# Performance work log

Measured on AMD Instinct MI355X. Metric: run time of the kernel, lower is better.

The kernel has to match this reference:

```python
import jax, jax.numpy as jnp
import numpy as np
from jax import lax

B, T = 1048576, 32
N_STATES, N_OBS = 3, 6


def setup_inputs() -> dict:
    key = jax.random.key(0)
    k1, k2, k3 = jax.random.split(key, 3)
    # probabilities in [0, 0.25) so that the '1 - sum' complement entries stay positive
    Y = jax.random.uniform(k1, (B, 13), dtype=jnp.float32) * 0.25
    obs = jax.random.randint(k2, (B, T), 0, N_OBS).astype(jnp.float32)
    lengths = jax.random.randint(k3, (B,), 4, T + 1)
    t_idx = jnp.arange(T)
    # NaN-pad the tail of each observation sequence (as in the original data format)
    Y_output = jnp.where(t_idx[None, :] < lengths[:, None], obs, jnp.nan)
    Pi_0 = jnp.ones((N_STATES,), dtype=jnp.int32)
    return {"Y": Y, "Y_output": Y_output, "Pi_0": Pi_0}


def _hmm_loss(Y, Y_output, Pi_0):
    b = Y.shape[0]
    t_len = Y_output.shape[1]
    Ysa = Y[:, :7]          # state-action chunk
    Yst = Y[:, 7:13]        # state chunk (6 used elements)
    z = jnp.zeros((b,), Y.dtype)
    # emission matrix [b, 3, 6] (faithful to original assignment order, incl. the
    # original bug: row 1 col 5 uses Y_state_action[1, 3] -- fixed batch index 1)
    row0 = jnp.stack([Ysa[:, 0], Ysa[:, 1], Ysa[:, 2],
                      1.0 - Ysa[:, 0] - Ysa[:, 1] - Ysa[:, 2], z, z], axis=-1)
    row1 = jnp.stack([z, z, z, z, Ysa[:, 3],
                      jnp.broadcast_to(1.0 - Ysa[1, 3], (b,))], axis=-1)
    row2 = jnp.stack([Ysa[:, 4], Ysa[:, 5], Ysa[:, 6],
                      1.0 - Ysa[:, 4] - Ysa[:, 5] - Ysa[:, 6], z, z], axis=-1)
    E = jnp.stack([row0, row1, row2], axis=1)            # [b, 3, 6]
    # transition matrix [b, 3, 3]
    Tm = Yst.reshape(b, 3, 2)
    Tr = jnp.concatenate([Tm, 1.0 - Tm.sum(-1, keepdims=True)], axis=-1)
    # sequence lengths: prefix up to first NaN
    nanmask = jnp.isnan(Y_output)
    lengths = jnp.where(nanmask.any(axis=1), jnp.argmax(nanmask, axis=1), t_len)
    obs = jnp.where(nanmask, 0.0, Y_output).astype(jnp.int32)  # [b, T]

    def emit(o):  # gather emission column: [b,3]
        return jnp.take_along_axis(E, o[:, None, None], axis=2)[:, :, 0]

    alpha = Pi_0.astype(E.dtype)[None, :] * emit(obs[:, 0])   # [b, 3]

    def step(alpha, inp):
        t, o = inp
        new = jnp.einsum('bj,bji->bi', alpha, Tr) * emit(o)
        alpha = jnp.where((t < lengths)[:, None], new, alpha)
        return alpha, None

    alpha, _ = lax.scan(step, alpha, (jnp.arange(1, t_len), obs.T[1:]))
    return jnp.sum(-jnp.log(alpha.sum(axis=1))) / b


def reference(Y, Y_output, Pi_0):
    return _hmm_loss(Y, Y_output, Pi_0)
```

## Files before the change

### kernel.cpp

```cpp
#include <hip/hip_runtime.h>

static constexpr int B_ROWS = 1048576;
static constexpr int T_LEN  = 32;
static constexpr int NTHR   = 256;
static constexpr int NCHUNK = B_ROWS / NTHR;
static constexpr int NBLK_MAX = 4096;

typedef float f32x4 __attribute__((ext_vector_type(4)));
typedef f32x4 f32x4_a4 __attribute__((aligned(4)));

__device__ __forceinline__ unsigned pk4(const float4 v) {
    const unsigned o0 = (unsigned)(int)fminf(v.x, 6.0f);
    const unsigned o1 = (unsigned)(int)fminf(v.y, 6.0f);
    const unsigned o2 = (unsigned)(int)fminf(v.z, 6.0f);
    const unsigned o3 = (unsigned)(int)fminf(v.w, 6.0f);
    return o0 | (o1 << 4) | (o2 << 8) | (o3 << 12);
}
#define OC(P, I) ((int)(((P) >> (4 * (I))) & 7u))

#define HMM_STEP(O) {                                                        \
    const float4 e = sE[(O)][threadIdx.x];                                   \
    const float n0 = (a0*t00 + a1*t10 + a2*t20) * e.x;                       \
    const float n1 = (a0*t01 + a1*t11 + a2*t21) * e.y;                       \
    const float n2 = (a0*t02 + a1*t12 + a2*t22) * e.z;                       \
    a0 = n0; a1 = n1; a2 = n2;                                               \
}

#define RESCALE {                                                            \
    const float s_ = a0 + a1 + a2;                                           \
    const bool sc = (s_ < 1e-2f);                                            \
    const float m_ = sc ? 0x1p20f : 1.0f;                                    \
    a0 *= m_; a1 *= m_; a2 *= m_;                                            \
    kk += sc ? 1 : 0;                                                        \
}

#define STEP2(A, B) HMM_STEP(A) HMM_STEP(B) RESCALE

__global__ __launch_bounds__(NTHR) void hmm_fwd_kernel(
    const float* __restrict__ Y,
    const float* __restrict__ Yo,
    const int*   __restrict__ Pi0,
    double*      __restrict__ partials,
    int nblk)
{
    __shared__ float4 sE[8][NTHR];

    const float fe15 = 1.0f - Y[1 * 13 + 3];
    const float pi0 = (float)Pi0[0];
    const float pi1 = (float)Pi0[1];
    const float pi2 = (float)Pi0[2];
    const int tid = threadIdx.x;

    double local = 0.0;
    for (int chunk = blockIdx.x; chunk < NCHUNK; chunk += nblk) {
        const int r = chunk * NTHR + tid;

        const float4* yo4 = reinterpret_cast<const float4*>(Yo + (size_t)r * T_LEN);
        const float4 v0 = yo4[0], v1 = yo4[1], v2 = yo4[2], v3 = yo4[3];
        const float4 v4 = yo4[4], v5 = yo4[5], v6 = yo4[6], v7 = yo4[7];
        const unsigned P0 = pk4(v0) | (pk4(v1) << 16);
        const unsigned P1 = pk4(v2) | (pk4(v3) << 16);
        const unsigned P2 = pk4(v4) | (pk4(v5) << 16);
        const unsigned P3 = pk4(v6) | (pk4(v7) << 16);

        const float* y = Y + (size_t)r * 13;
        const f32x4_a4 ya = *reinterpret_cast<const f32x4_a4*>(y + 0);
        const f32x4_a4 yb = *reinterpret_cast<const f32x4_a4*>(y + 4);
        const f32x4_a4 yc = *reinterpret_cast<const f32x4_a4*>(y + 8);
        const float    yd = y[12];
        const float fy0 = ya.x, fy1 = ya.y, fy2 = ya.z, fy3 = ya.w;
        const float fy4 = yb.x, fy5 = yb.y, fy6 = yb.z;
        const float fr03 = 1.0f - fy0 - fy1 - fy2;
        const float fr23 = 1.0f - fy4 - fy5 - fy6;
        const float t00 = yb.w, t01 = yc.x;
        const float t10 = yc.y, t11 = yc.z;
        const float t20 = yc.w, t21 = yd;
        const float t02 = 1.0f - t00 - t01;
        const float t12 = 1.0f - t10 - t11;
        const float t22 = 1.0f - t20 - t21;

        sE[0][tid] = make_float4(fy0,  0.0f, fy4,  0.0f);
        sE[1][tid] = make_float4(fy1,  0.0f, fy5,  0.0f);
        sE[2][tid] = make_float4(fy2,  0.0f, fy6,  0.0f);
        sE[3][tid] = make_float4(fr03, 0.0f, fr23, 0.0f);
        sE[4][tid] = make_float4(0.0f, fy3,  0.0f, 0.0f);
        sE[5][tid] = make_float4(0.0f, fe15, 0.0f, 0.0f);
        sE[6][tid] = make_float4(1.0f, 1.0f, 1.0f, 0.0f);

        float a0, a1, a2;
        {
            const float4 e = sE[OC(P0, 0)][tid];
            a0 = pi0 * e.x;
            a1 = pi1 * e.y;
            a2 = pi2 * e.z;
        }
        int kk = 0;

        HMM_STEP(OC(P0, 1))
        STEP2(OC(P0, 2), OC(P0, 3))
        STEP2(OC(P0, 4), OC(P0, 5))
        STEP2(OC(P0, 6), OC(P0, 7))
        STEP2(OC(P1, 0), OC(P1, 1))
        STEP2(OC(P1, 2), OC(P1, 3))
        STEP2(OC(P1, 4), OC(P1, 5))
        STEP2(OC(P1, 6), OC(P1, 7))
        STEP2(OC(P2, 0), OC(P2, 1))
        STEP2(OC(P2, 2), OC(P2, 3))
        STEP2(OC(P2, 4), OC(P2, 5))
        STEP2(OC(P2, 6), OC(P2, 7))
        STEP2(OC(P3, 0), OC(P3, 1))
        STEP2(OC(P3, 2), OC(P3, 3))
        STEP2(OC(P3, 4), OC(P3, 5))
        STEP2(OC(P3, 6), OC(P3, 7))

        float asum = a0 + a1 + a2;
        if (!(asum >= 1e-35f)) asum = 1e-35f;
        local += (double)logf(asum)
               - (double)kk * (20.0 * 0.6931471805599453);
    }

    #pragma unroll
    for (int off = 32; off > 0; off >>= 1)
        local += __shfl_down(local, off, 64);
    __shared__ double sred[NTHR / 64];
    const int lane = threadIdx.x & 63;
    const int wv   = threadIdx.x >> 6;
    if (lane == 0) sred[wv] = local;
    __syncthreads();
    if (threadIdx.x == 0) {
        double s = 0.0;
        #pragma unroll
        for (int i = 0; i < NTHR / 64; ++i) s += sred[i];
        partials[blockIdx.x] = s;
    }
}

__global__ __launch_bounds__(256) void hmm_final_kernel(
    const double* __restrict__ partials, float* __restrict__ out, int nblk)
{
    double local = 0.0;
    for (int i = threadIdx.x; i < nblk; i += 256) local += partials[i];
    #pragma unroll
    for (int off = 32; off > 0; off >>= 1)
        local += __shfl_down(local, off, 64);
    __shared__ double sred[4];
    const int lane = threadIdx.x & 63;
    const int wv   = threadIdx.x >> 6;
    if (lane == 0) sred[wv] = local;
    __syncthreads();
    if (threadIdx.x == 0) {
        double s = sred[0] + sred[1] + sred[2] + sred[3];
        out[0] = (float)(-s / (double)B_ROWS);
    }
}

extern "C" void kernel_launch(void* const* d_in, const int* in_sizes, int n_in,
                              void* d_out, int out_size, void* d_ws, size_t ws_size,
                              hipStream_t stream)
{
    const float* Y   = nullptr;
    const float* Yo  = nullptr;
    const int*   Pi0 = nullptr;
    for (int i = 0; i < n_in; ++i) {
        if (in_sizes[i] == B_ROWS * 13)      Y   = (const float*)d_in[i];
        else if (in_sizes[i] == B_ROWS * 32) Yo  = (const float*)d_in[i];
        else if (in_sizes[i] == 3)           Pi0 = (const int*)d_in[i];
    }

    int nblk = NBLK_MAX;
    if (ws_size < (size_t)NBLK_MAX * sizeof(double)) {
        nblk = (int)(ws_size / sizeof(double));
        if (nblk < 1) nblk = 1;
    }
    double* partials = (double*)d_ws;

    hmm_fwd_kernel<<<nblk, NTHR, 0, stream>>>(Y, Yo, Pi0, partials, nblk);
    hmm_final_kernel<<<1, 256, 0, stream>>>(partials, (float*)d_out, nblk);
}
```

Baseline: 39.71 us.

## Collapse 3-state HMM recurrence to 2-state pair-indexed transfer matrices

The 3-state forward recursion is replaced by a 2-variable recurrence that exploits the emission structure: state 1 is reachable only on observations 4/5, so pairs of (previous-obs class, obs) index precomputed 2x2 combined transition-emission matrices stored per thread in shared memory. This removes one state's FMAs per step and the per-step emission lookup of three values. The kernel also switches to one row per thread with 8192 blocks of 128 threads, dropping the grid-stride loop and the workspace-size check. The final reduction now reads 8192 partials, and correctness depends on the index-encoding tricks for NaN and state-1 transitions.

```diff
diff --git a/kernel.cpp b/kernel.cpp
--- a/kernel.cpp
+++ b/kernel.cpp
@@ -2,9 +2,9 @@
 
 static constexpr int B_ROWS = 1048576;
 static constexpr int T_LEN  = 32;
-static constexpr int NTHR   = 256;
-static constexpr int NCHUNK = B_ROWS / NTHR;
-static constexpr int NBLK_MAX = 4096;
+static constexpr int NTHR   = 128;
+static constexpr int NBLK   = B_ROWS / NTHR;
+static constexpr int TSTRIDE = 15;
 
 typedef float f32x4 __attribute__((ext_vector_type(4)));
 typedef f32x4 f32x4_a4 __attribute__((aligned(4)));
@@ -16,123 +16,141 @@
     const unsigned o3 = (unsigned)(int)fminf(v.w, 6.0f);
     return o0 | (o1 << 4) | (o2 << 8) | (o3 << 12);
 }
-#define OC(P, I) ((int)(((P) >> (4 * (I))) & 7u))
 
-#define HMM_STEP(O) {                                                        \
-    const float4 e = sE[(O)][threadIdx.x];                                   \
-    const float n0 = (a0*t00 + a1*t10 + a2*t20) * e.x;                       \
-    const float n1 = (a0*t01 + a1*t11 + a2*t21) * e.y;                       \
-    const float n2 = (a0*t02 + a1*t12 + a2*t22) * e.z;                       \
-    a0 = n0; a1 = n1; a2 = n2;                                               \
+#define STEPM(IDXW, T) {                                                     \
+    const int idx = (int)(((IDXW) >> (4 * (T))) & 15u);                      \
+    const f32x4 E = sM[tid15 + idx];                                         \
+    const float u_ = E.x * p, v_ = E.z * p;                                  \
+    p = fmaf(E.y, q, u_);                                                    \
+    q = fmaf(E.w, q, v_);                                                    \
 }
 
 #define RESCALE {                                                            \
-    const float s_ = a0 + a1 + a2;                                           \
+    const float s_ = p + q;                                                  \
     const bool sc = (s_ < 1e-2f);                                            \
     const float m_ = sc ? 0x1p20f : 1.0f;                                    \
-    a0 *= m_; a1 *= m_; a2 *= m_;                                            \
+    p *= m_; q *= m_;                                                        \
     kk += sc ? 1 : 0;                                                        \
 }
 
-#define STEP2(A, B) HMM_STEP(A) HMM_STEP(B) RESCALE
+#define STEPM2(W0, T0, W1, T1) STEPM(W0, T0) STEPM(W1, T1) RESCALE
 
 __global__ __launch_bounds__(NTHR) void hmm_fwd_kernel(
     const float* __restrict__ Y,
     const float* __restrict__ Yo,
     const int*   __restrict__ Pi0,
-    double*      __restrict__ partials,
-    int nblk)
+    double*      __restrict__ partials)
 {
-    __shared__ float4 sE[8][NTHR];
+    __shared__ f32x4 sM[NTHR * TSTRIDE];
 
     const float fe15 = 1.0f - Y[1 * 13 + 3];
     const float pi0 = (float)Pi0[0];
     const float pi1 = (float)Pi0[1];
     const float pi2 = (float)Pi0[2];
-    const int tid = threadIdx.x;
+    const int tid   = threadIdx.x;
+    const int tid15 = tid * TSTRIDE;
 
-    double local = 0.0;
-    for (int chunk = blockIdx.x; chunk < NCHUNK; chunk += nblk) {
-        const int r = chunk * NTHR + tid;
+    const int r = blockIdx.x * NTHR + tid;
 
-        const float4* yo4 = reinterpret_cast<const float4*>(Yo + (size_t)r * T_LEN);
-        const float4 v0 = yo4[0], v1 = yo4[1], v2 = yo4[2], v3 = yo4[3];
-        const float4 v4 = yo4[4], v5 = yo4[5], v6 = yo4[6], v7 = yo4[7];
-        const unsigned P0 = pk4(v0) | (pk4(v1) << 16);
-        const unsigned P1 = pk4(v2) | (pk4(v3) << 16);
-        const unsigned P2 = pk4(v4) | (pk4(v5) << 16);
-        const unsigned P3 = pk4(v6) | (pk4(v7) << 16);
+    const float4* yo4 = reinterpret_cast<const float4*>(Yo + (size_t)r * T_LEN);
+    const float4 w0 = yo4[0], w1 = yo4[1], w2 = yo4[2], w3 = yo4[3];
+    const float4 w4 = yo4[4], w5 = yo4[5], w6 = yo4[6], w7 = yo4[7];
+    const int o0 = (int)w0.x;
+    const unsigned P0 = pk4(w0) | (pk4(w1) << 16);
+    const unsigned P1 = pk4(w2) | (pk4(w3) << 16);
+    const unsigned P2 = pk4(w4) | (pk4(w5) << 16);
+    const unsigned P3 = pk4(w6) | (pk4(w7) << 16);
 
-        const float* y = Y + (size_t)r * 13;
-        const f32x4_a4 ya = *reinterpret_cast<const f32x4_a4*>(y + 0);
-        const f32x4_a4 yb = *reinterpret_cast<const f32x4_a4*>(y + 4);
-        const f32x4_a4 yc = *reinterpret_cast<const f32x4_a4*>(y + 8);
-        const float    yd = y[12];
-        const float fy0 = ya.x, fy1 = ya.y, fy2 = ya.z, fy3 = ya.w;
-        const float fy4 = yb.x, fy5 = yb.y, fy6 = yb.z;
-        const float fr03 = 1.0f - fy0 - fy1 - fy2;
-        const float fr23 = 1.0f - fy4 - fy5 - fy6;
-        const float t00 = yb.w, t01 = yc.x;
-        const float t10 = yc.y, t11 = yc.z;
-        const float t20 = yc.w, t21 = yd;
-        const float t02 = 1.0f - t00 - t01;
-        const float t12 = 1.0f - t10 - t11;
-        const float t22 = 1.0f - t20 - t21;
+    const unsigned PR0 = (P0 << 4);
+    const unsigned PR1 = (P1 << 4) | (P0 >> 28);
+    const unsigned PR2 = (P2 << 4) | (P1 >> 28);
+    const unsigned PR3 = (P3 << 4) | (P2 >> 28);
+    const unsigned G0 = (PR0 >> 2) & 0x11111111u;
+    const unsigned G1 = (PR1 >> 2) & 0x11111111u;
+    const unsigned G2 = (PR2 >> 2) & 0x11111111u;
+    const unsigned G3 = (PR3 >> 2) & 0x11111111u;
+    const unsigned I0 = P0 + (G0 << 3) - G0;
+    const unsigned I1 = P1 + (G1 << 3) - G1;
+    const unsigned I2 = P2 + (G2 << 3) - G2;
+    const unsigned I3 = P3 + (G3 << 3) - G3;
 
-        sE[0][tid] = make_float4(fy0,  0.0f, fy4,  0.0f);
-        sE[1][tid] = make_float4(fy1,  0.0f, fy5,  0.0f);
-        sE[2][tid] = make_float4(fy2,  0.0f, fy6,  0.0f);
-        sE[3][tid] = make_float4(fr03, 0.0f, fr23, 0.0f);
-        sE[4][tid] = make_float4(0.0f, fy3,  0.0f, 0.0f);
-        sE[5][tid] = make_float4(0.0f, fe15, 0.0f, 0.0f);
-        sE[6][tid] = make_float4(1.0f, 1.0f, 1.0f, 0.0f);
+    const float* y = Y + (size_t)r * 13;
+    const f32x4_a4 ya = *reinterpret_cast<const f32x4_a4*>(y + 0);
+    const f32x4_a4 yb = *reinterpret_cast<const f32x4_a4*>(y + 4);
+    const f32x4_a4 yc = *reinterpret_cast<const f32x4_a4*>(y + 8);
+    const float    yd = y[12];
+    const float fy0 = ya.x, fy1 = ya.y, fy2 = ya.z, fy3 = ya.w;
+    const float fy4 = yb.x, fy5 = yb.y, fy6 = yb.z;
+    const float fr03 = 1.0f - fy0 - fy1 - fy2;
+    const float fr23 = 1.0f - fy4 - fy5 - fy6;
+    const float t00 = yb.w, t01 = yc.x;
+    const float t10 = yc.y, t11 = yc.z;
+    const float t20 = yc.w, t21 = yd;
+    const float t02 = 1.0f - t00 - t01;
+    const float t12 = 1.0f - t10 - t11;
+    const float t22 = 1.0f - t20 - t21;
 
-        float a0, a1, a2;
-        {
-            const float4 e = sE[OC(P0, 0)][tid];
-            a0 = pi0 * e.x;
-            a1 = pi1 * e.y;
-            a2 = pi2 * e.z;
-        }
-        int kk = 0;
+    {
+        f32x4 e;
+        e.x = t00*fy0;  e.y = t20*fy0;  e.z = t02*fy4;  e.w = t22*fy4;  sM[tid15+0]  = e;
+        e.x = t00*fy1;  e.y = t20*fy1;  e.z = t02*fy5;  e.w = t22*fy5;  sM[tid15+1]  = e;
+        e.x = t00*fy2;  e.y = t20*fy2;  e.z = t02*fy6;  e.w = t22*fy6;  sM[tid15+2]  = e;
+        e.x = t00*fr03; e.y = t20*fr03; e.z = t02*fr23; e.w = t22*fr23; sM[tid15+3]  = e;
+        e.x = t01*fy3;  e.y = t21*fy3;  e.z = 0.0f;     e.w = 0.0f;     sM[tid15+4]  = e;
+        e.x = t01*fe15; e.y = t21*fe15; e.z = 0.0f;     e.w = 0.0f;     sM[tid15+5]  = e;
+        e.x = 1.0f;     e.y = 0.0f;     e.z = 0.0f;     e.w = 1.0f;     sM[tid15+6]  = e;
+        e.x = t10*fy0;  e.y = 0.0f;     e.z = t12*fy4;  e.w = 0.0f;     sM[tid15+7]  = e;
+        e.x = t10*fy1;  e.y = 0.0f;     e.z = t12*fy5;  e.w = 0.0f;     sM[tid15+8]  = e;
+        e.x = t10*fy2;  e.y = 0.0f;     e.z = t12*fy6;  e.w = 0.0f;     sM[tid15+9]  = e;
+        e.x = t10*fr03; e.y = 0.0f;     e.z = t12*fr23; e.w = 0.0f;     sM[tid15+10] = e;
+        e.x = t11*fy3;  e.y = 0.0f;     e.z = 0.0f;     e.w = 0.0f;     sM[tid15+11] = e;
+        e.x = t11*fe15; e.y = 0.0f;     e.z = 0.0f;     e.w = 0.0f;     sM[tid15+12] = e;
+        e.x = 1.0f;     e.y = 0.0f;     e.z = 0.0f;     e.w = 1.0f;     sM[tid15+13] = e;
+    }
 
-        HMM_STEP(OC(P0, 1))
-        STEP2(OC(P0, 2), OC(P0, 3))
-        STEP2(OC(P0, 4), OC(P0, 5))
-        STEP2(OC(P0, 6), OC(P0, 7))
-        STEP2(OC(P1, 0), OC(P1, 1))
-        STEP2(OC(P1, 2), OC(P1, 3))
-        STEP2(OC(P1, 4), OC(P1, 5))
-        STEP2(OC(P1, 6), OC(P1, 7))
-        STEP2(OC(P2, 0), OC(P2, 1))
-        STEP2(OC(P2, 2), OC(P2, 3))
-        STEP2(OC(P2, 4), OC(P2, 5))
-        STEP2(OC(P2, 6), OC(P2, 7))
-        STEP2(OC(P3, 0), OC(P3, 1))
-        STEP2(OC(P3, 2), OC(P3, 3))
-        STEP2(OC(P3, 4), OC(P3, 5))
-        STEP2(OC(P3, 6), OC(P3, 7))
+    float p, q;
+    {
+        const float e0i = (o0==0)?fy0:(o0==1)?fy1:(o0==2)?fy2:fr03;
+        const float e2i = (o0==0)?fy4:(o0==1)?fy5:(o0==2)?fy6:fr23;
+        const float e1i = (o0==4)?fy3:fe15;
+        const bool m0 = (o0 >= 4);
+        p = m0 ? pi1 * e1i : pi0 * e0i;
+        q = m0 ? 0.0f      : pi2 * e2i;
+    }
+    int kk = 0;
 
-        float asum = a0 + a1 + a2;
-        if (!(asum >= 1e-35f)) asum = 1e-35f;
-        local += (double)logf(asum)
-               - (double)kk * (20.0 * 0.6931471805599453);
-    }
+    STEPM(I0, 1)
+    STEPM2(I0, 2, I0, 3)
+    STEPM2(I0, 4, I0, 5)
+    STEPM2(I0, 6, I0, 7)
+    STEPM2(I1, 0, I1, 1)
+    STEPM2(I1, 2, I1, 3)
+    STEPM2(I1, 4, I1, 5)
+    STEPM2(I1, 6, I1, 7)
+    STEPM2(I2, 0, I2, 1)
+    STEPM2(I2, 2, I2, 3)
+    STEPM2(I2, 4, I2, 5)
+    STEPM2(I2, 6, I2, 7)
+    STEPM2(I3, 0, I3, 1)
+    STEPM2(I3, 2, I3, 3)
+    STEPM2(I3, 4, I3, 5)
+    STEPM2(I3, 6, I3, 7)
+
+    float s = p + q;
+    if (!(s >= 1e-35f)) s = 1e-35f;
+    double local = (double)logf(s)
+                 - (double)kk * (20.0 * 0.6931471805599453);
 
     #pragma unroll
     for (int off = 32; off > 0; off >>= 1)
         local += __shfl_down(local, off, 64);
     __shared__ double sred[NTHR / 64];
-    const int lane = threadIdx.x & 63;
-    const int wv   = threadIdx.x >> 6;
+    const int lane = tid & 63;
+    const int wv   = tid >> 6;
     if (lane == 0) sred[wv] = local;
     __syncthreads();
-    if (threadIdx.x == 0) {
-        double s = 0.0;
-        #pragma unroll
-        for (int i = 0; i < NTHR / 64; ++i) s += sred[i];
-        partials[blockIdx.x] = s;
-    }
+    if (tid == 0)
+        partials[blockIdx.x] = sred[0] + sred[1];
 }
 
 __global__ __launch_bounds__(256) void hmm_final_kernel(
@@ -167,13 +185,8 @@
         else if (in_sizes[i] == 3)           Pi0 = (const int*)d_in[i];
     }
 
-    int nblk = NBLK_MAX;
-    if (ws_size < (size_t)NBLK_MAX * sizeof(double)) {
-        nblk = (int)(ws_size / sizeof(double));
-        if (nblk < 1) nblk = 1;
-    }
     double* partials = (double*)d_ws;
 
-    hmm_fwd_kernel<<<nblk, NTHR, 0, stream>>>(Y, Yo, Pi0, partials, nblk);
-    hmm_final_kernel<<<1, 256, 0, stream>>>(partials, (float*)d_out, nblk);
+    hmm_fwd_kernel<<<NBLK, NTHR, 0, stream>>>(Y, Yo, Pi0, partials);
+    hmm_final_kernel<<<1, 256, 0, stream>>>(partials, (float*)d_out, NBLK);
 }
```

After: 45.03 us. 1.13x slower.
